# Performance work log

Hardware: AMD Instinct MI355X
Metric: run time of the kernel (lower is better)

Reference implementation:

```python
import jax, jax.numpy as jnp
import numpy as np

C = 4096      # n_channels (total blocks)
B = 2048      # active blocks (len(indices))
T = 1024      # coords per block
DIN, DH, DOUT = 3, 64, 3
OMEGA0 = 30.0


def setup_inputs() -> dict:
    key = jax.random.key(0)
    ks = jax.random.split(key, 12)
    inp = jax.random.normal(ks[0], (C, T, DIN), dtype=jnp.float32)
    indices = jax.random.randint(ks[1], (B,), 0, C)
    # SIREN init: first layer uniform(-1/in, 1/in); hidden uniform(-sqrt(6/in)/w0, ...)
    b_first = 1.0 / DIN
    b_hid = float(np.sqrt(6.0 / DH) / OMEGA0)
    b_last = float(np.sqrt(1.0 / DH) / OMEGA0)
    u = lambda k, shape, b: jax.random.uniform(k, shape, jnp.float32, -b, b)
    return {
        "inp": inp, "indices": indices,
        "W0": u(ks[2], (C, DIN, DH), b_first), "b0": u(ks[3], (C, 1, DH), b_first),
        "W1": u(ks[4], (C, DH, DH), b_hid),   "b1": u(ks[5], (C, 1, DH), b_hid),
        "W2": u(ks[6], (C, DH, DH), b_hid),   "b2": u(ks[7], (C, 1, DH), b_hid),
        "W3": u(ks[8], (C, DH, DOUT), b_last), "b3": u(ks[9], (C, 1, DOUT), b_last),
    }


def _adaptive_linear(x, W, b, idx):
    # gather per-active-block weights then batched matmul: [B,T,i] @ [B,i,o] + [B,1,o]
    return jnp.einsum('bti,bio->bto', x, W[idx]) + b[idx]


def reference(inp, indices, W0, b0, W1, b1, W2, b2, W3, b3):
    x = inp[indices]                                     # [B,T,DIN]
    x = jnp.sin(OMEGA0 * _adaptive_linear(x, W0, b0, indices))
    x = jnp.sin(OMEGA0 * _adaptive_linear(x, W1, b1, indices))
    x = jnp.sin(OMEGA0 * _adaptive_linear(x, W2, b2, indices))
    x = _adaptive_linear(x, W3, b3, indices)             # outermost linear
    return x                                             # [B,T,DOUT]
```

## Files before the change

kernel.cpp:

```cpp
#include <hip/hip_runtime.h>
#include <hip/hip_bf16.h>


namespace {

constexpr int   TPTS = 1024;
constexpr float C30  = 30.0f * 0.15915494309189535f;

typedef float        f32x4 __attribute__((ext_vector_type(4)));
typedef short        s16x8 __attribute__((ext_vector_type(8)));
typedef unsigned int u32x4 __attribute__((ext_vector_type(4)));
typedef unsigned int u32x2 __attribute__((ext_vector_type(2)));

__device__ __forceinline__ unsigned short bfr(float x) {
    __hip_bfloat16 h = __float2bfloat16(x);
    unsigned short u;
    __builtin_memcpy(&u, &h, sizeof(u));
    return u;
}
__device__ __forceinline__ float bf2f(unsigned short u) {
    unsigned int w = (unsigned int)u << 16;
    float f;
    __builtin_memcpy(&f, &w, sizeof(f));
    return f;
}
__device__ __forceinline__ float sin_rev(float r) {
    return __builtin_amdgcn_sinf(__builtin_amdgcn_fractf(r));
}

__device__ __forceinline__ void act_store(const f32x4 (&acc)[4][2],
                                          unsigned char* lh,
                                          int tw, int l15, int kg) {
    const unsigned swz = (unsigned)(l15 & 7) << 4;
    #pragma unroll
    for (int ni = 0; ni < 4; ++ni) {
        #pragma unroll
        for (int tj = 0; tj < 2; ++tj) {
            f32x4 a = acc[ni][tj];
            unsigned short s0 = bfr(sin_rev(a[0]));
            unsigned short s1 = bfr(sin_rev(a[1]));
            unsigned short s2 = bfr(sin_rev(a[2]));
            unsigned short s3 = bfr(sin_rev(a[3]));
            u32x2 p;
            p[0] = (unsigned)s0 | ((unsigned)s1 << 16);
            p[1] = (unsigned)s2 | ((unsigned)s3 << 16);
            const int trow = tw + tj * 16 + l15;
            *(u32x2*)(lh + trow * 128 +
                      (((unsigned)(ni * 32 + kg * 8)) ^ swz)) = p;
        }
    }
}

__device__ __forceinline__ void hidden_layer(f32x4 (&acc)[4][2],
                                             const unsigned char* lw,
                                             const unsigned char* lh,
                                             const float* lb,
                                             int tw, int l15, int kg) {
    const unsigned swz = (unsigned)(l15 & 7) << 4;
    #pragma unroll
    for (int ni = 0; ni < 4; ++ni) {
        f32x4 bv = *(const f32x4*)(lb + ni * 16 + kg * 4);
        #pragma unroll
        for (int tj = 0; tj < 2; ++tj) acc[ni][tj] = bv;
    }
    #pragma unroll
    for (int ks = 0; ks < 2; ++ks) {
        const unsigned ko = (unsigned)(ks * 64 + kg * 16);
        s16x8 wf[4], hf[2];
        #pragma unroll
        for (int ni = 0; ni < 4; ++ni)
            wf[ni] = *(const s16x8*)(lw + (ni * 16 + l15) * 128 + (ko ^ swz));
        #pragma unroll
        for (int tj = 0; tj < 2; ++tj)
            hf[tj] = *(const s16x8*)(lh + (tw + tj * 16 + l15) * 128 + (ko ^ swz));
        #pragma unroll
        for (int ni = 0; ni < 4; ++ni) {
            #pragma unroll
            for (int tj = 0; tj < 2; ++tj)
                acc[ni][tj] = __builtin_amdgcn_mfma_f32_16x16x32_bf16(
                    wf[ni], hf[tj], acc[ni][tj], 0, 0, 0);
        }
    }
}

}

__global__ __launch_bounds__(256, 4) void siren_fused(
    const float* __restrict__ inp, const int* __restrict__ indices,
    const float* __restrict__ W0, const float* __restrict__ b0,
    const float* __restrict__ W1, const float* __restrict__ b1,
    const float* __restrict__ W2, const float* __restrict__ b2,
    const float* __restrict__ W3, const float* __restrict__ b3,
    float* __restrict__ out)
{
    __shared__ __align__(16) unsigned char lds[37632];
    unsigned char* const lh  = lds;
    unsigned char* const lw1 = lds + 16384;
    unsigned char* const lw2 = lds + 24576;
    unsigned char* const lw3 = lds + 32768;
    unsigned char* const lw0 = lds + 34816;
    float*         const lbias = (float*)(lds + 36864);

    const int tid  = threadIdx.x;
    const int lane = tid & 63;
    const int wid  = tid >> 6;
    const int l15  = lane & 15;
    const int kg   = lane >> 4;
    const int bid  = blockIdx.x;

    const int idx = __builtin_amdgcn_readfirstlane(indices[bid]);

    const float* const W0g = W0 + (size_t)idx * 192;
    const float* const b0g = b0 + (size_t)idx * 64;
    const float* const W1g = W1 + (size_t)idx * 4096;
    const float* const b1g = b1 + (size_t)idx * 64;
    const float* const W2g = W2 + (size_t)idx * 4096;
    const float* const b2g = b2 + (size_t)idx * 64;
    const float* const W3g = W3 + (size_t)idx * 192;
    const float* const b3g = b3 + (size_t)idx * 3;

    {
        const int n  = tid & 63;
        const int kc = (tid >> 6) * 16;
        const unsigned rowb = (unsigned)n * 128u;
        const unsigned swzn = (unsigned)(n & 7) << 4;
        #pragma unroll
        for (int w = 0; w < 2; ++w) {
            const float* Wg = w ? W2g : W1g;
            unsigned char* lw = w ? lw2 : lw1;
            unsigned int q[8];
            #pragma unroll
            for (int j = 0; j < 8; ++j) {
                unsigned short e0 = bfr(Wg[(kc + 2 * j    ) * 64 + n] * C30);
                unsigned short e1 = bfr(Wg[(kc + 2 * j + 1) * 64 + n] * C30);
                q[j] = (unsigned)e0 | ((unsigned)e1 << 16);
            }
            u32x4 q0 = {q[0], q[1], q[2], q[3]};
            u32x4 q1 = {q[4], q[5], q[6], q[7]};
            *(u32x4*)(lw + rowb + (((unsigned)(kc * 2)      ) ^ swzn)) = q0;
            *(u32x4*)(lw + rowb + (((unsigned)(kc * 2) + 16u) ^ swzn)) = q1;
        }
        if (tid < 192) {
            const int g = tid >> 6, o = tid & 63;
            const float* bg = (g == 0) ? b0g : (g == 1) ? b1g : b2g;
            lbias[tid] = bg[o] * C30;
        }
        if (tid < 208) {
            u32x2 z; z[0] = 0u; z[1] = 0u;
            *(u32x2*)(lw3 + 384 + tid * 8) = z;
        }
        if (tid < 64) {
            const int k = tid;
            #pragma unroll
            for (int c = 0; c < 3; ++c) {
                unsigned short v = bfr(W3g[k * 3 + c]);
                *(unsigned short*)(lw3 + (unsigned)c * 128u +
                                   (((unsigned)(2 * k)) ^ ((unsigned)c << 4))) = v;
            }
            unsigned short wh[3], wl[3];
            #pragma unroll
            for (int i = 0; i < 3; ++i) {
                float ws = W0g[i * 64 + k] * C30;
                wh[i] = bfr(ws);
                wl[i] = bfr(ws - bf2f(wh[i]));
            }
            u32x4 r0 = { (unsigned)wh[0] | ((unsigned)wh[1] << 16),
                         (unsigned)wh[2],
                         (unsigned)wh[0] | ((unsigned)wh[1] << 16),
                         (unsigned)wh[2] };
            u32x4 r1 = { (unsigned)wl[0] | ((unsigned)wl[1] << 16),
                         (unsigned)wl[2], 0u, 0u };
            *(u32x4*)(lw0 + k * 32)      = r0;
            *(u32x4*)(lw0 + k * 32 + 16) = r1;
        }
    }
    __syncthreads();

    const float* const xg = inp + (size_t)idx * (TPTS * 3);
    float*       const og = out + (size_t)bid * (TPTS * 3);
    const int tw = wid * 32;
    const unsigned swz = (unsigned)(l15 & 7) << 4;

    #pragma unroll 1
    for (int tile = 0; tile < 8; ++tile) {
        const int tbase = tile * 128 + tw;

        s16x8 xf[2];
        #pragma unroll
        for (int tj = 0; tj < 2; ++tj) {
            const float* xr = xg + (size_t)(tbase + tj * 16 + l15) * 3;
            float x0 = xr[0], x1 = xr[1], x2 = xr[2];
            unsigned short h0 = bfr(x0), h1 = bfr(x1), h2 = bfr(x2);
            unsigned short g0 = bfr(x0 - bf2f(h0));
            unsigned short g1 = bfr(x1 - bf2f(h1));
            unsigned short g2 = bfr(x2 - bf2f(h2));
            const bool hi = (kg < 2), lo = (kg == 0);
            s16x8 v;
            v[0] = hi ? (short)h0 : (short)0;
            v[1] = hi ? (short)h1 : (short)0;
            v[2] = hi ? (short)h2 : (short)0;
            v[3] = 0;
            v[4] = lo ? (short)g0 : (short)0;
            v[5] = lo ? (short)g1 : (short)0;
            v[6] = lo ? (short)g2 : (short)0;
            v[7] = 0;
            xf[tj] = v;
        }
        f32x4 acc[4][2];
        #pragma unroll
        for (int ni = 0; ni < 4; ++ni) {
            f32x4 bv = *(const f32x4*)(lbias + ni * 16 + kg * 4);
            #pragma unroll
            for (int tj = 0; tj < 2; ++tj) acc[ni][tj] = bv;
        }
        #pragma unroll
        for (int ni = 0; ni < 4; ++ni) {
            const s16x8 wf = *(const s16x8*)(lw0 + (ni * 16 + l15) * 32 + (kg & 1) * 16);
            #pragma unroll
            for (int tj = 0; tj < 2; ++tj)
                acc[ni][tj] = __builtin_amdgcn_mfma_f32_16x16x32_bf16(
                    wf, xf[tj], acc[ni][tj], 0, 0, 0);
        }
        act_store(acc, lh, tw, l15, kg);

        hidden_layer(acc, lw1, lh, lbias + 64, tw, l15, kg);
        act_store(acc, lh, tw, l15, kg);
        hidden_layer(acc, lw2, lh, lbias + 128, tw, l15, kg);
        act_store(acc, lh, tw, l15, kg);

        {
            const float bb0 = b3g[0], bb1 = b3g[1], bb2 = b3g[2];
            f32x4 acc3[2];
            #pragma unroll
            for (int tj = 0; tj < 2; ++tj) {
                f32x4 c; c[0] = bb0; c[1] = bb1; c[2] = bb2; c[3] = 0.0f;
                acc3[tj] = c;
            }
            #pragma unroll
            for (int ks = 0; ks < 2; ++ks) {
                const unsigned ko = (unsigned)(ks * 64 + kg * 16);
                const s16x8 wf = *(const s16x8*)(lw3 + l15 * 128 + (ko ^ swz));
                #pragma unroll
                for (int tj = 0; tj < 2; ++tj) {
                    const s16x8 hf = *(const s16x8*)(lh + (tw + tj * 16 + l15) * 128 + (ko ^ swz));
                    acc3[tj] = __builtin_amdgcn_mfma_f32_16x16x32_bf16(
                        wf, hf, acc3[tj], 0, 0, 0);
                }
            }
            if (kg == 0) {
                #pragma unroll
                for (int tj = 0; tj < 2; ++tj) {
                    float* o = og + (size_t)(tbase + tj * 16 + l15) * 3;
                    o[0] = acc3[tj][0];
                    o[1] = acc3[tj][1];
                    o[2] = acc3[tj][2];
                }
            }
        }
    }
}

extern "C" void kernel_launch(void* const* d_in, const int* in_sizes, int n_in,
                              void* d_out, int out_size, void* d_ws, size_t ws_size,
                              hipStream_t stream) {
    (void)in_sizes; (void)n_in; (void)out_size; (void)d_ws; (void)ws_size;
    siren_fused<<<dim3(2048), dim3(256), 0, stream>>>(
        (const float*)d_in[0], (const int*)d_in[1],
        (const float*)d_in[2], (const float*)d_in[3],
        (const float*)d_in[4], (const float*)d_in[5],
        (const float*)d_in[6], (const float*)d_in[7],
        (const float*)d_in[8], (const float*)d_in[9],
        (float*)d_out);
}
```

Baseline: 249.2 us.

## Hoist hidden-layer weight fragments into registers and fold layer-0 bias into MFMA

W1 and W2 bf16 fragments are loaded from LDS once per block into registers (16 s16x8 vectors per lane) instead of being reloaded every tile, which cuts LDS read traffic in the hidden layers. The first-layer bias is folded into the MFMA as an extra input column fixed to 1.0, with hi/lo bf16 split bias weights, so the accumulator starts at zero and layer-0 bias LDS storage and loads go away. The cost is extra VGPR pressure, which with launch_bounds(256,4) may cause spills or limit occupancy.

```diff
diff --git a/kernel.cpp b/kernel.cpp
--- a/kernel.cpp
+++ b/kernel.cpp
@@ -52,7 +52,7 @@
 }
 
 __device__ __forceinline__ void hidden_layer(f32x4 (&acc)[4][2],
-                                             const unsigned char* lw,
+                                             const s16x8 (&wf)[2][4],
                                              const unsigned char* lh,
                                              const float* lb,
                                              int tw, int l15, int kg) {
@@ -66,10 +66,7 @@
     #pragma unroll
     for (int ks = 0; ks < 2; ++ks) {
         const unsigned ko = (unsigned)(ks * 64 + kg * 16);
-        s16x8 wf[4], hf[2];
-        #pragma unroll
-        for (int ni = 0; ni < 4; ++ni)
-            wf[ni] = *(const s16x8*)(lw + (ni * 16 + l15) * 128 + (ko ^ swz));
+        s16x8 hf[2];
         #pragma unroll
         for (int tj = 0; tj < 2; ++tj)
             hf[tj] = *(const s16x8*)(lh + (tw + tj * 16 + l15) * 128 + (ko ^ swz));
@@ -78,7 +75,7 @@
             #pragma unroll
             for (int tj = 0; tj < 2; ++tj)
                 acc[ni][tj] = __builtin_amdgcn_mfma_f32_16x16x32_bf16(
-                    wf[ni], hf[tj], acc[ni][tj], 0, 0, 0);
+                    wf[ks][ni], hf[tj], acc[ni][tj], 0, 0, 0);
         }
     }
 }
@@ -93,7 +90,7 @@
     const float* __restrict__ W3, const float* __restrict__ b3,
     float* __restrict__ out)
 {
-    __shared__ __align__(16) unsigned char lds[37632];
+    __shared__ __align__(16) unsigned char lds[37376];
     unsigned char* const lh  = lds;
     unsigned char* const lw1 = lds + 16384;
     unsigned char* const lw2 = lds + 24576;
@@ -140,9 +137,9 @@
             *(u32x4*)(lw + rowb + (((unsigned)(kc * 2)      ) ^ swzn)) = q0;
             *(u32x4*)(lw + rowb + (((unsigned)(kc * 2) + 16u) ^ swzn)) = q1;
         }
-        if (tid < 192) {
+        if (tid < 128) {
             const int g = tid >> 6, o = tid & 63;
-            const float* bg = (g == 0) ? b0g : (g == 1) ? b1g : b2g;
+            const float* bg = g ? b2g : b1g;
             lbias[tid] = bg[o] * C30;
         }
         if (tid < 208) {
@@ -164,10 +161,13 @@
                 wh[i] = bfr(ws);
                 wl[i] = bfr(ws - bf2f(wh[i]));
             }
+            const float bs = b0g[k] * C30;
+            unsigned short Bhi = bfr(bs);
+            unsigned short Blo = bfr(bs - bf2f(Bhi));
             u32x4 r0 = { (unsigned)wh[0] | ((unsigned)wh[1] << 16),
-                         (unsigned)wh[2],
+                         (unsigned)wh[2] | ((unsigned)Bhi   << 16),
                          (unsigned)wh[0] | ((unsigned)wh[1] << 16),
-                         (unsigned)wh[2] };
+                         (unsigned)wh[2] | ((unsigned)Blo   << 16) };
             u32x4 r1 = { (unsigned)wl[0] | ((unsigned)wl[1] << 16),
                          (unsigned)wl[2], 0u, 0u };
             *(u32x4*)(lw0 + k * 32)      = r0;
@@ -176,10 +176,22 @@
     }
     __syncthreads();
 
+    const unsigned swz = (unsigned)(l15 & 7) << 4;
+
+    s16x8 w1r[2][4], w2r[2][4];
+    #pragma unroll
+    for (int ks = 0; ks < 2; ++ks) {
+        const unsigned ko = (unsigned)(ks * 64 + kg * 16);
+        #pragma unroll
+        for (int ni = 0; ni < 4; ++ni) {
+            w1r[ks][ni] = *(const s16x8*)(lw1 + (ni * 16 + l15) * 128 + (ko ^ swz));
+            w2r[ks][ni] = *(const s16x8*)(lw2 + (ni * 16 + l15) * 128 + (ko ^ swz));
+        }
+    }
+
     const float* const xg = inp + (size_t)idx * (TPTS * 3);
     float*       const og = out + (size_t)bid * (TPTS * 3);
     const int tw = wid * 32;
-    const unsigned swz = (unsigned)(l15 & 7) << 4;
 
     #pragma unroll 1
     for (int tile = 0; tile < 8; ++tile) {
@@ -195,23 +207,26 @@
             unsigned short g1 = bfr(x1 - bf2f(h1));
             unsigned short g2 = bfr(x2 - bf2f(h2));
             const bool hi = (kg < 2), lo = (kg == 0);
+            const short one = lo ? (short)0x3F80 : (short)0;
             s16x8 v;
             v[0] = hi ? (short)h0 : (short)0;
             v[1] = hi ? (short)h1 : (short)0;
             v[2] = hi ? (short)h2 : (short)0;
-            v[3] = 0;
+            v[3] = one;
             v[4] = lo ? (short)g0 : (short)0;
             v[5] = lo ? (short)g1 : (short)0;
             v[6] = lo ? (short)g2 : (short)0;
-            v[7] = 0;
+            v[7] = one;
             xf[tj] = v;
         }
         f32x4 acc[4][2];
         #pragma unroll
         for (int ni = 0; ni < 4; ++ni) {
-            f32x4 bv = *(const f32x4*)(lbias + ni * 16 + kg * 4);
-            #pragma unroll
-            for (int tj = 0; tj < 2; ++tj) acc[ni][tj] = bv;
+            #pragma unroll
+            for (int tj = 0; tj < 2; ++tj) {
+                f32x4 z; z[0] = 0.f; z[1] = 0.f; z[2] = 0.f; z[3] = 0.f;
+                acc[ni][tj] = z;
+            }
         }
         #pragma unroll
         for (int ni = 0; ni < 4; ++ni) {
@@ -223,9 +238,9 @@
         }
         act_store(acc, lh, tw, l15, kg);
 
-        hidden_layer(acc, lw1, lh, lbias + 64, tw, l15, kg);
+        hidden_layer(acc, w1r, lh, lbias,      tw, l15, kg);
         act_store(acc, lh, tw, l15, kg);
-        hidden_layer(acc, lw2, lh, lbias + 128, tw, l15, kg);
+        hidden_layer(acc, w2r, lh, lbias + 64, tw, l15, kg);
         act_store(acc, lh, tw, l15, kg);
 
         {
```

New measurement: 248.1 us. Within noise of the previous version (-0.4%).
